# Kernel tuning notes

Measured on AMD Instinct MI355X. Metric: run time of the kernel, lower is better.

The kernel has to match this reference:

```python
import jax, jax.numpy as jnp
import numpy as np

B = 16
H = 56
W = 56
C = 384
NH = 12
HD = C // NH
WS = 7
SHIFT = 3
N = WS * WS
SCALE = HD ** -0.5
EPS = 1e-3  # keras LayerNormalization default epsilon


def _rel_pos_index():
    coords = np.stack(np.meshgrid(np.arange(WS), np.arange(WS), indexing='ij')).reshape(2, -1)
    rel = (coords[:, :, None] - coords[:, None, :]).transpose(1, 2, 0)
    rel[:, :, 0] += WS - 1
    rel[:, :, 1] += WS - 1
    rel[:, :, 0] *= 2 * WS - 1
    return rel.sum(-1)  # [N, N]

REL_IDX = jnp.asarray(_rel_pos_index())


def _shift_mask():
    # faithful reproduction of the TransformerBlock.__init__ mask construction
    mask = np.zeros((1, H, W, 1), np.float32)
    slices = (slice(0, -WS), slice(-WS, -SHIFT), slice(-SHIFT, None))
    cnt = 0
    for hs in slices:
        for ws in slices:
            mask[:, hs, ws, :] = cnt
            cnt += 1
    mw = mask.reshape(1, H // WS, WS, W // WS, WS, 1).transpose(0, 1, 3, 2, 4, 5).reshape(-1, N)
    m = mw[:, None, :] - mw[:, :, None]  # expand_dims(mw,1) - expand_dims(mw,2)
    return np.where(m != 0, np.float32(-100.0), np.float32(0.0))  # [nw, N, N]

MASK = jnp.asarray(_shift_mask())


def _ln(x, g, b):
    mu = x.mean(-1, keepdims=True)
    var = ((x - mu) ** 2).mean(-1, keepdims=True)
    return (x - mu) / jnp.sqrt(var + EPS) * g + b


def _window_partition(x):  # [B,H,W,C] -> [B*nw, N, C]
    b = x.shape[0]
    x = x.reshape(b, H // WS, WS, W // WS, WS, C).transpose(0, 1, 3, 2, 4, 5)
    return x.reshape(-1, N, C)


def _window_reverse(wins, b):  # [B*nw, WS, WS, C] -> [B,H,W,C]
    x = wins.reshape(b, H // WS, W // WS, WS, WS, C).transpose(0, 1, 3, 2, 4, 5)
    return x.reshape(b, H, W, C)


def setup_inputs() -> dict:
    key = jax.random.key(0)
    ks = jax.random.split(key, 8)
    s = 0.02
    return {
        'x': jax.random.normal(ks[0], (B, H * W, C), jnp.float32),
        'ln1_g': jnp.ones((C,), jnp.float32),
        'ln1_b': jnp.zeros((C,), jnp.float32),
        'ln2_g': jnp.ones((C,), jnp.float32),
        'ln2_b': jnp.zeros((C,), jnp.float32),
        'qkv_w': s * jax.random.normal(ks[1], (C, 3 * C), jnp.float32),
        'qkv_b': jnp.zeros((3 * C,), jnp.float32),
        'proj_w': s * jax.random.normal(ks[2], (C, C), jnp.float32),
        'proj_b': jnp.zeros((C,), jnp.float32),
        'mlp_w1': s * jax.random.normal(ks[3], (C, 4 * C), jnp.float32),
        'mlp_b1': jnp.zeros((4 * C,), jnp.float32),
        'mlp_w2': s * jax.random.normal(ks[4], (4 * C, C), jnp.float32),
        'mlp_b2': jnp.zeros((C,), jnp.float32),
        'rel_pos_table': s * jax.random.normal(ks[5], ((2 * WS - 1) * (2 * WS - 1), NH), jnp.float32),
    }


def reference(x, ln1_g, ln1_b, ln2_g, ln2_b, qkv_w, qkv_b, proj_w, proj_b,
              mlp_w1, mlp_b1, mlp_w2, mlp_b2, rel_pos_table):
    skip = x
    y = _ln(x, ln1_g, ln1_b).reshape(B, H, W, C)
    # cyclic shift (faithful to source: shift=(-s, +s))
    y = jnp.roll(y, shift=(-SHIFT, SHIFT), axis=(1, 2))
    wins = _window_partition(y)                      # [nW, N, C]
    nW = wins.shape[0]

    qkv = wins @ qkv_w + qkv_b                       # [nW, N, 3C]
    qkv = qkv.reshape(nW, N, 3, NH, HD).transpose(2, 0, 3, 1, 4)
    q, k, v = qkv[0] * SCALE, qkv[1], qkv[2]         # [nW, NH, N, HD]

    attn = jnp.einsum('whnd,whmd->whnm', q, k)       # [nW, NH, N, N]
    bias = rel_pos_table[REL_IDX.reshape(-1)].reshape(N, N, NH).transpose(2, 0, 1)
    attn = attn + bias[None]

    nw = MASK.shape[0]
    attn = attn.reshape(nW // nw, nw, NH, N, N) + MASK[None, :, None]
    attn = jax.nn.softmax(attn.reshape(nW, NH, N, N), axis=-1)

    out = jnp.einsum('whnm,whmd->wnhd', attn, v).reshape(nW, N, C)
    out = out @ proj_w + proj_b

    y = _window_reverse(out.reshape(-1, WS, WS, C), B)
    # reverse shift (faithful to source: shift=(+s, +s))
    y = jnp.roll(y, shift=(SHIFT, SHIFT), axis=(1, 2))
    x = y.reshape(B, H * W, C) + skip

    skip = x
    y = _ln(x, ln2_g, ln2_b)
    y = jax.nn.gelu(y @ mlp_w1 + mlp_b1, approximate=False)
    y = y @ mlp_w2 + mlp_b2
    return y + skip
```

## Files before the change

### kernel.cpp

```cpp
#include <hip/hip_runtime.h>
#include <hip/hip_bf16.h>
#include <math.h>

typedef __hip_bfloat16 bf16;
typedef unsigned short ushort_t;
typedef __bf16 bf16x8 __attribute__((ext_vector_type(8)));
typedef float f32x4 __attribute__((ext_vector_type(4)));

#define TOKENS 50176
#define CW2 512
#define CROWS2 (CW2 * 49)
#define SCALE_ 0.17677669529663687f

__device__ __forceinline__ float b2f(bf16 v) { return __bfloat162float(v); }
__device__ __forceinline__ bf16  f2b(float v) { return __float2bfloat16(v); }

__device__ __forceinline__ float gelu_f(float v) {
  float x = v * 0.7071067811865475f;
  float ax = fabsf(x);
  float t = 1.f / (1.f + 0.3275911f * ax);
  float poly = ((((1.061405429f * t - 1.453152027f) * t + 1.421413741f) * t
                 - 0.284496736f) * t + 0.254829592f) * t;
  float erfv = 1.f - poly * __expf(-ax * ax);
  erfv = copysignf(erfv, x);
  return 0.5f * v * (1.f + erfv);
}

__global__ __launch_bounds__(256) void wt_bf16(const float* __restrict__ W,
                                               ushort_t* __restrict__ Wt,
                                               int K, int N) {
  int idx = blockIdx.x * 256 + threadIdx.x;
  if (idx >= K * N) return;
  int n = idx / K, k = idx - n * K;
  bf16 h = f2b(W[(size_t)k * N + n]);
  Wt[idx] = *(ushort_t*)&h;
}

__global__ __launch_bounds__(64) void ln1_kernel(const float* __restrict__ x,
                                                 const float* __restrict__ g,
                                                 const float* __restrict__ bta,
                                                 bf16* __restrict__ wins) {
  int t = blockIdx.x;
  int lane = threadIdx.x;
  int w = t / 49, n = t - w * 49;
  int bi = w >> 6, wi = w & 63;
  int hw = wi >> 3, ww = wi & 7;
  int ti = n / 7, tj = n - ti * 7;
  int hr = hw * 7 + ti, wr = ww * 7 + tj;
  int hs = (hr + 3) % 56;
  int wsc = (wr + 53) % 56;
  const float* row = x + ((size_t)bi * 3136 + hs * 56 + wsc) * 384;
  float v[6];
  float s = 0.f, s2 = 0.f;
#pragma unroll
  for (int j = 0; j < 6; ++j) {
    v[j] = row[lane + 64 * j];
    s += v[j]; s2 += v[j] * v[j];
  }
#pragma unroll
  for (int m = 32; m >= 1; m >>= 1) {
    s  += __shfl_xor(s, m, 64);
    s2 += __shfl_xor(s2, m, 64);
  }
  float mu = s * (1.f / 384.f);
  float var = s2 * (1.f / 384.f) - mu * mu;
  float rstd = rsqrtf(var + 1e-3f);
  bf16* orow = wins + (size_t)t * 384;
#pragma unroll
  for (int j = 0; j < 6; ++j) {
    int c = lane + 64 * j;
    orow[c] = f2b((v[j] - mu) * rstd * g[c] + bta[c]);
  }
}

__global__ __launch_bounds__(64) void ln2_kernel(const float* __restrict__ x1,
                                                 const float* __restrict__ g,
                                                 const float* __restrict__ bta,
                                                 bf16* __restrict__ out) {
  int t = blockIdx.x;
  int lane = threadIdx.x;
  const float* row = x1 + (size_t)t * 384;
  float v[6];
  float s = 0.f, s2 = 0.f;
#pragma unroll
  for (int j = 0; j < 6; ++j) {
    v[j] = row[lane + 64 * j];
    s += v[j]; s2 += v[j] * v[j];
  }
#pragma unroll
  for (int m = 32; m >= 1; m >>= 1) {
    s  += __shfl_xor(s, m, 64);
    s2 += __shfl_xor(s2, m, 64);
  }
  float mu = s * (1.f / 384.f);
  float var = s2 * (1.f / 384.f) - mu * mu;
  float rstd = rsqrtf(var + 1e-3f);
  bf16* orow = out + (size_t)t * 384;
#pragma unroll
  for (int j = 0; j < 6; ++j) {
    int c = lane + 64 * j;
    orow[c] = f2b((v[j] - mu) * rstd * g[c] + bta[c]);
  }
}

template<int MODE>
__global__ __launch_bounds__(256) void mfma_gemm(
    const ushort_t* __restrict__ A, const ushort_t* __restrict__ Bt,
    const float* __restrict__ bias, int N, int K,
    const float* __restrict__ resid, void* __restrict__ out_) {
  __shared__ ushort_t As[2][128 * 32];
  __shared__ ushort_t Bs[2][128 * 32];
  int tid = threadIdx.x;
  int lane = tid & 63, wv = tid >> 6;
  int wm = wv >> 1, wn = wv & 1;
  int lm = lane & 15, kg = lane >> 4;
  int col0 = blockIdx.x * 128, row0 = blockIdx.y * 128;
  f32x4 acc[4][4];
#pragma unroll
  for (int i = 0; i < 4; ++i)
#pragma unroll
    for (int j = 0; j < 4; ++j) acc[i][j] = (f32x4){0.f, 0.f, 0.f, 0.f};

  int rsub = lane >> 2;
  int bs = (lane & 3) ^ ((rsub >> 1) & 3);
  int pbr = kg ^ ((lm >> 1) & 3);

  auto stage = [&](int t, int buf) {
    int kk0 = t << 5;
#pragma unroll
    for (int ch = 0; ch < 2; ++ch) {
      int c = wv * 2 + ch;
      int r = c * 16 + rsub;
      const ushort_t* ga = &A[(size_t)(row0 + r) * K + kk0 + bs * 8];
      const ushort_t* gb = &Bt[(size_t)(col0 + r) * K + kk0 + bs * 8];
      __builtin_amdgcn_global_load_lds(
          (const __attribute__((address_space(1))) void*)ga,
          (__attribute__((address_space(3))) void*)&As[buf][c * 512], 16, 0, 0);
      __builtin_amdgcn_global_load_lds(
          (const __attribute__((address_space(1))) void*)gb,
          (__attribute__((address_space(3))) void*)&Bs[buf][c * 512], 16, 0, 0);
    }
  };

  int NT = K >> 5;
  int cur = 0;
  stage(0, 0);
  __syncthreads();

  for (int t = 0; t < NT; ++t) {
    if (t + 1 < NT) stage(t + 1, cur ^ 1);
    bf16x8 a[4], b[4];
#pragma unroll
    for (int i = 0; i < 4; ++i) {
      int ra = wm * 64 + i * 16 + lm;
      int rb = wn * 64 + i * 16 + lm;
      a[i] = *(const bf16x8*)&As[cur][ra * 32 + pbr * 8];
      b[i] = *(const bf16x8*)&Bs[cur][rb * 32 + pbr * 8];
    }
#pragma unroll
    for (int i = 0; i < 4; ++i)
#pragma unroll
      for (int j = 0; j < 4; ++j)
        acc[i][j] = __builtin_amdgcn_mfma_f32_16x16x32_bf16(a[i], b[j], acc[i][j], 0, 0, 0);
    __syncthreads();
    cur ^= 1;
  }

  int m0 = row0 + wm * 64, n0 = col0 + wn * 64;
#pragma unroll
  for (int i = 0; i < 4; ++i) {
#pragma unroll
    for (int reg = 0; reg < 4; ++reg) {
      int m = m0 + i * 16 + kg * 4 + reg;
      size_t obase = 0;
      if (MODE == 1) {
        int w = m / 49, nn = m - w * 49;
        int bi = w >> 6, wi = w & 63;
        int hw = wi >> 3, ww = wi & 7;
        int ti = nn / 7, tj = nn - ti * 7;
        int hf = (hw * 7 + ti + 3) % 56, wf = (ww * 7 + tj + 3) % 56;
        obase = ((size_t)bi * 3136 + hf * 56 + wf) * 384;
      }
#pragma unroll
      for (int j = 0; j < 4; ++j) {
        int cN = n0 + j * 16 + lm;
        float v = acc[i][j][reg] + bias[cN];
        if (MODE == 0) {
          ((bf16*)out_)[(size_t)m * N + cN] = f2b(v);
        } else if (MODE == 1) {
          float* O = (float*)out_;
          O[obase + cN] = v + resid[obase + cN];
        } else if (MODE == 2) {
          ((bf16*)out_)[(size_t)m * N + cN] = f2b(gelu_f(v));
        } else {
          float* O = (float*)out_;
          O[(size_t)m * N + cN] = v + resid[(size_t)m * N + cN];
        }
      }
    }
  }
}

__global__ __launch_bounds__(256) void attn_mfma(const ushort_t* __restrict__ qkv_c,
                                                 const float* __restrict__ table,
                                                 ushort_t* __restrict__ attn_c,
                                                 int w_base) {
  int wl = blockIdx.x >> 2, hg = blockIdx.x & 3;
  int w = w_base + wl;
  int wi = w & 63;
  int hw = wi >> 3, ww = wi & 7;
  __shared__ ushort_t Qs[64 * 40];
  __shared__ ushort_t Ks[64 * 40];
  __shared__ ushort_t Vt[32 * 72];
  __shared__ ushort_t Ps[64 * 72];
  __shared__ float bias_s[169 * 12];
  int tid = threadIdx.x;
  int lane = tid & 63, wv = tid >> 6;
  int lm = lane & 15, kg = lane >> 4;

  for (int i = tid; i < 64 * 40; i += 256) { Qs[i] = 0; Ks[i] = 0; }
  for (int i = tid; i < 32 * 72; i += 256) Vt[i] = 0;
  for (int i = tid; i < 169 * 12; i += 256) bias_s[i] = table[i];
  __syncthreads();

  for (int hh = 0; hh < 3; ++hh) {
    int h = hg * 3 + hh;
    const ushort_t* base = qkv_c + (size_t)wl * 49 * 1152 + h * 32;
    for (int idx = tid; idx < 392; idx += 256) {
      int n = idx >> 3, d0 = (idx & 7) * 4;
      const ushort_t* p = base + (size_t)n * 1152 + d0;
      ushort4 q = *(const ushort4*)(p);
      ushort4 k = *(const ushort4*)(p + 384);
      ushort4 v = *(const ushort4*)(p + 768);
      *(ushort4*)&Qs[n * 40 + d0] = q;
      *(ushort4*)&Ks[n * 40 + d0] = k;
      Vt[(d0 + 0) * 72 + n] = v.x;
      Vt[(d0 + 1) * 72 + n] = v.y;
      Vt[(d0 + 2) * 72 + n] = v.z;
      Vt[(d0 + 3) * 72 + n] = v.w;
    }
    __syncthreads();

    bf16x8 qa = *(const bf16x8*)&Qs[(wv * 16 + lm) * 40 + kg * 8];
    f32x4 sacc[4];
#pragma unroll
    for (int jt = 0; jt < 4; ++jt) {
      bf16x8 kb = *(const bf16x8*)&Ks[(jt * 16 + lm) * 40 + kg * 8];
      sacc[jt] = __builtin_amdgcn_mfma_f32_16x16x32_bf16(
          qa, kb, (f32x4){0.f, 0.f, 0.f, 0.f}, 0, 0, 0);
    }

    int i_base = wv * 16 + kg * 4;
#pragma unroll
    for (int reg = 0; reg < 4; ++reg) {
      int i = i_base + reg;
      int ii = (i < 49) ? i : 0;
      int yi = ii / 7, xi = ii - yi * 7;
      int hri = hw * 7 + yi, wri = ww * 7 + xi;
      int ri = (hri < 49 ? 0 : (hri < 53 ? 1 : 2)) * 3 + (wri < 49 ? 0 : (wri < 53 ? 1 : 2));
      float sv[4];
      float mx = -1e30f;
#pragma unroll
      for (int jt = 0; jt < 4; ++jt) {
        int j = jt * 16 + lm;
        int jj = (j < 49) ? j : 0;
        int yj = jj / 7, xj = jj - yj * 7;
        int hrj = hw * 7 + yj, wrj = ww * 7 + xj;
        int rj = (hrj < 49 ? 0 : (hrj < 53 ? 1 : 2)) * 3 + (wrj < 49 ? 0 : (wrj < 53 ? 1 : 2));
        int ridx = (yi - yj + 6) * 13 + (xi - xj + 6);
        float s = sacc[jt][reg] * SCALE_ + bias_s[ridx * 12 + h] + ((ri == rj) ? 0.f : -100.f);
        sv[jt] = (j < 49) ? s : -1e30f;
        mx = fmaxf(mx, sv[jt]);
      }
#pragma unroll
      for (int msk = 1; msk < 16; msk <<= 1) mx = fmaxf(mx, __shfl_xor(mx, msk, 64));
      float sm = 0.f;
#pragma unroll
      for (int jt = 0; jt < 4; ++jt) {
        float e = ((jt * 16 + lm) < 49) ? __expf(sv[jt] - mx) : 0.f;
        sv[jt] = e; sm += e;
      }
#pragma unroll
      for (int msk = 1; msk < 16; msk <<= 1) sm += __shfl_xor(sm, msk, 64);
      float inv = 1.f / sm;
#pragma unroll
      for (int jt = 0; jt < 4; ++jt) {
        bf16 pb = f2b(sv[jt] * inv);
        Ps[(size_t)i * 72 + jt * 16 + lm] = *(ushort_t*)&pb;
      }
    }
    f32x4 oacc[2] = {(f32x4){0.f, 0.f, 0.f, 0.f}, (f32x4){0.f, 0.f, 0.f, 0.f}};
#pragma unroll
    for (int ks = 0; ks < 2; ++ks) {
      bf16x8 pa = *(const bf16x8*)&Ps[(wv * 16 + lm) * 72 + ks * 32 + kg * 8];
#pragma unroll
      for (int dt = 0; dt < 2; ++dt) {
        bf16x8 vb = *(const bf16x8*)&Vt[(dt * 16 + lm) * 72 + ks * 32 + kg * 8];
        oacc[dt] = __builtin_amdgcn_mfma_f32_16x16x32_bf16(pa, vb, oacc[dt], 0, 0, 0);
      }
    }
#pragma unroll
    for (int reg = 0; reg < 4; ++reg) {
      int r = i_base + reg;
      if (r < 49) {
#pragma unroll
        for (int dt = 0; dt < 2; ++dt) {
          bf16 ob = f2b(oacc[dt][reg]);
          attn_c[((size_t)wl * 49 + r) * 384 + h * 32 + dt * 16 + lm] = *(ushort_t*)&ob;
        }
      }
    }
    __syncthreads();
  }
}

extern "C" void kernel_launch(void* const* d_in, const int* in_sizes, int n_in,
                              void* d_out, int out_size, void* d_ws, size_t ws_size,
                              hipStream_t stream) {
  const float* x      = (const float*)d_in[0];
  const float* ln1_g  = (const float*)d_in[1];
  const float* ln1_b  = (const float*)d_in[2];
  const float* ln2_g  = (const float*)d_in[3];
  const float* ln2_b  = (const float*)d_in[4];
  const float* qkv_w  = (const float*)d_in[5];
  const float* qkv_b  = (const float*)d_in[6];
  const float* proj_w = (const float*)d_in[7];
  const float* proj_b = (const float*)d_in[8];
  const float* mlp_w1 = (const float*)d_in[9];
  const float* mlp_b1 = (const float*)d_in[10];
  const float* mlp_w2 = (const float*)d_in[11];
  const float* mlp_b2 = (const float*)d_in[12];
  const float* rel_tb = (const float*)d_in[13];

  char* ws = (char*)d_ws;
  ushort_t* r0 = (ushort_t*)(ws + 0);
  ushort_t* r1 = (ushort_t*)(ws + 38535168ull);
  ushort_t* wq = (ushort_t*)(ws + 115605504ull);
  ushort_t* wp = wq + 442368;
  ushort_t* w1 = wp + 147456;
  ushort_t* w2 = w1 + 589824;
  float* out = (float*)d_out;

  wt_bf16<<<1728, 256, 0, stream>>>(qkv_w, wq, 384, 1152);
  wt_bf16<<<576, 256, 0, stream>>>(proj_w, wp, 384, 384);
  wt_bf16<<<2304, 256, 0, stream>>>(mlp_w1, w1, 384, 1536);
  wt_bf16<<<2304, 256, 0, stream>>>(mlp_w2, w2, 1536, 384);

  ln1_kernel<<<TOKENS, 64, 0, stream>>>(x, ln1_g, ln1_b, (bf16*)r0);

  for (int c = 0; c < 2; ++c) {
    ushort_t* winc = r0 + (size_t)c * CROWS2 * 384;
    mfma_gemm<0><<<dim3(9, CROWS2 / 128), 256, 0, stream>>>(
        winc, wq, qkv_b, 1152, 384, nullptr, (void*)r1);
    attn_mfma<<<CW2 * 4, 256, 0, stream>>>(r1, rel_tb, winc, c * CW2);
  }

  mfma_gemm<1><<<dim3(3, TOKENS / 128), 256, 0, stream>>>(
      r0, wp, proj_b, 384, 384, x, (void*)out);

  ln2_kernel<<<TOKENS, 64, 0, stream>>>(out, ln2_g, ln2_b, (bf16*)r0);

  for (int c = 0; c < 2; ++c) {
    ushort_t* lc = r0 + (size_t)c * CROWS2 * 384;
    float* oc = out + (size_t)c * CROWS2 * 384;
    mfma_gemm<2><<<dim3(12, CROWS2 / 128), 256, 0, stream>>>(
        lc, w1, mlp_b1, 1536, 384, nullptr, (void*)r1);
    mfma_gemm<3><<<dim3(3, CROWS2 / 128), 256, 0, stream>>>(
        r1, w2, mlp_b2, 384, 1536, oc, (void*)oc);
  }
}
```

Measured before the change: 668.5 us.

## Triple-buffer GEMM LDS pipeline and remap blocks for XCD-aware locality

The MFMA GEMM moves from a double-buffered to a triple-buffered LDS pipeline. Loads are issued two K-tiles ahead, and it waits with a partial vmcnt instead of draining, so there is one barrier per iteration. Launch now uses a 1D grid, and block IDs are remapped so consecutive tiles land on the same XCD, which is meant to improve L2 reuse of the shared A rows. The costs are 50% more LDS per block, which may lower occupancy, and reliance on hand-tuned waitcnt counts.

```diff
diff --git a/kernel.cpp b/kernel.cpp
--- a/kernel.cpp
+++ b/kernel.cpp
@@ -108,13 +108,20 @@
     const ushort_t* __restrict__ A, const ushort_t* __restrict__ Bt,
     const float* __restrict__ bias, int N, int K,
     const float* __restrict__ resid, void* __restrict__ out_) {
-  __shared__ ushort_t As[2][128 * 32];
-  __shared__ ushort_t Bs[2][128 * 32];
+  __shared__ ushort_t As[3][128 * 32];
+  __shared__ ushort_t Bs[3][128 * 32];
   int tid = threadIdx.x;
   int lane = tid & 63, wv = tid >> 6;
   int wm = wv >> 1, wn = wv & 1;
   int lm = lane & 15, kg = lane >> 4;
-  int col0 = blockIdx.x * 128, row0 = blockIdx.y * 128;
+
+  int nwg = gridDim.x;
+  int q = nwg >> 3, r = nwg & 7;
+  int xcd = blockIdx.x & 7, ii = blockIdx.x >> 3;
+  int l = ((xcd < r) ? xcd * (q + 1) : r * (q + 1) + (xcd - r) * q) + ii;
+  int nxt = N >> 7;
+  int col0 = (l % nxt) * 128, row0 = (l / nxt) * 128;
+
   f32x4 acc[4][4];
 #pragma unroll
   for (int i = 0; i < 4; ++i)
@@ -122,7 +129,7 @@
     for (int j = 0; j < 4; ++j) acc[i][j] = (f32x4){0.f, 0.f, 0.f, 0.f};
 
   int rsub = lane >> 2;
-  int bs = (lane & 3) ^ ((rsub >> 1) & 3);
+  int bsrc = (lane & 3) ^ ((rsub >> 1) & 3);
   int pbr = kg ^ ((lm >> 1) & 3);
 
   auto stage = [&](int t, int buf) {
@@ -130,9 +137,9 @@
 #pragma unroll
     for (int ch = 0; ch < 2; ++ch) {
       int c = wv * 2 + ch;
-      int r = c * 16 + rsub;
-      const ushort_t* ga = &A[(size_t)(row0 + r) * K + kk0 + bs * 8];
-      const ushort_t* gb = &Bt[(size_t)(col0 + r) * K + kk0 + bs * 8];
+      int rr = c * 16 + rsub;
+      const ushort_t* ga = &A[(size_t)(row0 + rr) * K + kk0 + bsrc * 8];
+      const ushort_t* gb = &Bt[(size_t)(col0 + rr) * K + kk0 + bsrc * 8];
       __builtin_amdgcn_global_load_lds(
           (const __attribute__((address_space(1))) void*)ga,
           (__attribute__((address_space(3))) void*)&As[buf][c * 512], 16, 0, 0);
@@ -142,29 +149,37 @@
     }
   };
 
-  int NT = K >> 5;
-  int cur = 0;
-  stage(0, 0);
-  __syncthreads();
-
-  for (int t = 0; t < NT; ++t) {
-    if (t + 1 < NT) stage(t + 1, cur ^ 1);
+  auto compute = [&](int buf) {
     bf16x8 a[4], b[4];
 #pragma unroll
     for (int i = 0; i < 4; ++i) {
       int ra = wm * 64 + i * 16 + lm;
       int rb = wn * 64 + i * 16 + lm;
-      a[i] = *(const bf16x8*)&As[cur][ra * 32 + pbr * 8];
-      b[i] = *(const bf16x8*)&Bs[cur][rb * 32 + pbr * 8];
+      a[i] = *(const bf16x8*)&As[buf][ra * 32 + pbr * 8];
+      b[i] = *(const bf16x8*)&Bs[buf][rb * 32 + pbr * 8];
     }
 #pragma unroll
     for (int i = 0; i < 4; ++i)
 #pragma unroll
       for (int j = 0; j < 4; ++j)
         acc[i][j] = __builtin_amdgcn_mfma_f32_16x16x32_bf16(a[i], b[j], acc[i][j], 0, 0, 0);
-    __syncthreads();
-    cur ^= 1;
-  }
+  };
+
+  int NT = K >> 5;
+  stage(0, 0);
+  stage(1, 1);
+
+  for (int t = 0; t < NT - 1; ++t) {
+    asm volatile("s_waitcnt vmcnt(4)" ::: "memory");
+    __builtin_amdgcn_sched_barrier(0);
+    __builtin_amdgcn_s_barrier();
+    if (t + 2 < NT) stage(t + 2, (t + 2) % 3);
+    compute(t % 3);
+  }
+  asm volatile("s_waitcnt vmcnt(0)" ::: "memory");
+  __builtin_amdgcn_sched_barrier(0);
+  __builtin_amdgcn_s_barrier();
+  compute((NT - 1) % 3);
 
   int m0 = row0 + wm * 64, n0 = col0 + wn * 64;
 #pragma unroll
@@ -350,12 +365,12 @@
 
   for (int c = 0; c < 2; ++c) {
     ushort_t* winc = r0 + (size_t)c * CROWS2 * 384;
-    mfma_gemm<0><<<dim3(9, CROWS2 / 128), 256, 0, stream>>>(
+    mfma_gemm<0><<<9 * (CROWS2 / 128), 256, 0, stream>>>(
         winc, wq, qkv_b, 1152, 384, nullptr, (void*)r1);
     attn_mfma<<<CW2 * 4, 256, 0, stream>>>(r1, rel_tb, winc, c * CW2);
   }
 
-  mfma_gemm<1><<<dim3(3, TOKENS / 128), 256, 0, stream>>>(
+  mfma_gemm<1><<<3 * (TOKENS / 128), 256, 0, stream>>>(
       r0, wp, proj_b, 384, 384, x, (void*)out);
 
   ln2_kernel<<<TOKENS, 64, 0, stream>>>(out, ln2_g, ln2_b, (bf16*)r0);
@@ -363,9 +378,9 @@
   for (int c = 0; c < 2; ++c) {
     ushort_t* lc = r0 + (size_t)c * CROWS2 * 384;
     float* oc = out + (size_t)c * CROWS2 * 384;
-    mfma_gemm<2><<<dim3(12, CROWS2 / 128), 256, 0, stream>>>(
+    mfma_gemm<2><<<12 * (CROWS2 / 128), 256, 0, stream>>>(
         lc, w1, mlp_b1, 1536, 384, nullptr, (void*)r1);
-    mfma_gemm<3><<<dim3(3, CROWS2 / 128), 256, 0, stream>>>(
+    mfma_gemm<3><<<3 * (CROWS2 / 128), 256, 0, stream>>>(
         r1, w2, mlp_b2, 384, 1536, oc, (void*)oc);
   }
 }
```

After: 686.0 us. 1.03x slower.

## Use 512-thread single-buffered GEMM blocks with XCD-aware tile remapping

Applied to the files above, without the earlier changes.

The MFMA GEMM now runs 8 waves per 128x128 tile, each computing 32x64 instead of 64x64, so per-thread accumulators halve and more waves fit per CU. LDS double buffering is dropped in favour of a single buffer with a sync after each load, relying on the higher occupancy to hide latency. Tiles are launched on a 1D grid and remapped so consecutive tiles land on the same XCD, to improve L2 reuse. The load-then-sync pattern loses any overlap inside a block, which can hurt if occupancy does not actually rise.

```diff
diff --git a/kernel.cpp b/kernel.cpp
--- a/kernel.cpp
+++ b/kernel.cpp
@@ -104,71 +104,68 @@
 }
 
 template<int MODE>
-__global__ __launch_bounds__(256) void mfma_gemm(
+__global__ __launch_bounds__(512, 6) void mfma_gemm(
     const ushort_t* __restrict__ A, const ushort_t* __restrict__ Bt,
     const float* __restrict__ bias, int N, int K,
     const float* __restrict__ resid, void* __restrict__ out_) {
-  __shared__ ushort_t As[2][128 * 32];
-  __shared__ ushort_t Bs[2][128 * 32];
+  __shared__ ushort_t As[128 * 32];
+  __shared__ ushort_t Bs[128 * 32];
   int tid = threadIdx.x;
   int lane = tid & 63, wv = tid >> 6;
   int wm = wv >> 1, wn = wv & 1;
   int lm = lane & 15, kg = lane >> 4;
-  int col0 = blockIdx.x * 128, row0 = blockIdx.y * 128;
-  f32x4 acc[4][4];
-#pragma unroll
-  for (int i = 0; i < 4; ++i)
+
+  int nwg = gridDim.x;
+  int q = nwg >> 3, r = nwg & 7;
+  int xcd = blockIdx.x & 7, ii = blockIdx.x >> 3;
+  int l = ((xcd < r) ? xcd * (q + 1) : r * (q + 1) + (xcd - r) * q) + ii;
+  int nxt = N >> 7;
+  int col0 = (l % nxt) * 128, row0 = (l / nxt) * 128;
+
+  f32x4 acc[2][4];
+#pragma unroll
+  for (int i = 0; i < 2; ++i)
 #pragma unroll
     for (int j = 0; j < 4; ++j) acc[i][j] = (f32x4){0.f, 0.f, 0.f, 0.f};
 
   int rsub = lane >> 2;
-  int bs = (lane & 3) ^ ((rsub >> 1) & 3);
+  int bsrc = (lane & 3) ^ ((rsub >> 1) & 3);
   int pbr = kg ^ ((lm >> 1) & 3);
 
-  auto stage = [&](int t, int buf) {
-    int kk0 = t << 5;
-#pragma unroll
-    for (int ch = 0; ch < 2; ++ch) {
-      int c = wv * 2 + ch;
-      int r = c * 16 + rsub;
-      const ushort_t* ga = &A[(size_t)(row0 + r) * K + kk0 + bs * 8];
-      const ushort_t* gb = &Bt[(size_t)(col0 + r) * K + kk0 + bs * 8];
-      __builtin_amdgcn_global_load_lds(
-          (const __attribute__((address_space(1))) void*)ga,
-          (__attribute__((address_space(3))) void*)&As[buf][c * 512], 16, 0, 0);
-      __builtin_amdgcn_global_load_lds(
-          (const __attribute__((address_space(1))) void*)gb,
-          (__attribute__((address_space(3))) void*)&Bs[buf][c * 512], 16, 0, 0);
-    }
-  };
+  const ushort_t* gA = &A[(size_t)(row0 + wv * 16 + rsub) * K + bsrc * 8];
+  const ushort_t* gB = &Bt[(size_t)(col0 + wv * 16 + rsub) * K + bsrc * 8];
 
   int NT = K >> 5;
-  int cur = 0;
-  stage(0, 0);
-  __syncthreads();
-
   for (int t = 0; t < NT; ++t) {
-    if (t + 1 < NT) stage(t + 1, cur ^ 1);
-    bf16x8 a[4], b[4];
-#pragma unroll
-    for (int i = 0; i < 4; ++i) {
-      int ra = wm * 64 + i * 16 + lm;
-      int rb = wn * 64 + i * 16 + lm;
-      a[i] = *(const bf16x8*)&As[cur][ra * 32 + pbr * 8];
-      b[i] = *(const bf16x8*)&Bs[cur][rb * 32 + pbr * 8];
-    }
-#pragma unroll
-    for (int i = 0; i < 4; ++i)
+    __builtin_amdgcn_global_load_lds(
+        (const __attribute__((address_space(1))) void*)(gA + (t << 5)),
+        (__attribute__((address_space(3))) void*)&As[wv * 512], 16, 0, 0);
+    __builtin_amdgcn_global_load_lds(
+        (const __attribute__((address_space(1))) void*)(gB + (t << 5)),
+        (__attribute__((address_space(3))) void*)&Bs[wv * 512], 16, 0, 0);
+    __syncthreads();
+    bf16x8 a[2], b[4];
+#pragma unroll
+    for (int i = 0; i < 2; ++i) {
+      int ra = wm * 32 + i * 16 + lm;
+      a[i] = *(const bf16x8*)&As[ra * 32 + pbr * 8];
+    }
+#pragma unroll
+    for (int j = 0; j < 4; ++j) {
+      int rb = wn * 64 + j * 16 + lm;
+      b[j] = *(const bf16x8*)&Bs[rb * 32 + pbr * 8];
+    }
+#pragma unroll
+    for (int i = 0; i < 2; ++i)
 #pragma unroll
       for (int j = 0; j < 4; ++j)
         acc[i][j] = __builtin_amdgcn_mfma_f32_16x16x32_bf16(a[i], b[j], acc[i][j], 0, 0, 0);
     __syncthreads();
-    cur ^= 1;
-  }
-
-  int m0 = row0 + wm * 64, n0 = col0 + wn * 64;
-#pragma unroll
-  for (int i = 0; i < 4; ++i) {
+  }
+
+  int m0 = row0 + wm * 32, n0 = col0 + wn * 64;
+#pragma unroll
+  for (int i = 0; i < 2; ++i) {
 #pragma unroll
     for (int reg = 0; reg < 4; ++reg) {
       int m = m0 + i * 16 + kg * 4 + reg;
@@ -350,12 +347,12 @@
 
   for (int c = 0; c < 2; ++c) {
     ushort_t* winc = r0 + (size_t)c * CROWS2 * 384;
-    mfma_gemm<0><<<dim3(9, CROWS2 / 128), 256, 0, stream>>>(
+    mfma_gemm<0><<<(CROWS2 / 128) * 9, 512, 0, stream>>>(
         winc, wq, qkv_b, 1152, 384, nullptr, (void*)r1);
     attn_mfma<<<CW2 * 4, 256, 0, stream>>>(r1, rel_tb, winc, c * CW2);
   }
 
-  mfma_gemm<1><<<dim3(3, TOKENS / 128), 256, 0, stream>>>(
+  mfma_gemm<1><<<(TOKENS / 128) * 3, 512, 0, stream>>>(
       r0, wp, proj_b, 384, 384, x, (void*)out);
 
   ln2_kernel<<<TOKENS, 64, 0, stream>>>(out, ln2_g, ln2_b, (bf16*)r0);
@@ -363,9 +360,9 @@
   for (int c = 0; c < 2; ++c) {
     ushort_t* lc = r0 + (size_t)c * CROWS2 * 384;
     float* oc = out + (size_t)c * CROWS2 * 384;
-    mfma_gemm<2><<<dim3(12, CROWS2 / 128), 256, 0, stream>>>(
+    mfma_gemm<2><<<(CROWS2 / 128) * 12, 512, 0, stream>>>(
         lc, w1, mlp_b1, 1536, 384, nullptr, (void*)r1);
-    mfma_gemm<3><<<dim3(3, CROWS2 / 128), 256, 0, stream>>>(
+    mfma_gemm<3><<<(CROWS2 / 128) * 3, 512, 0, stream>>>(
         r1, w2, mlp_b2, 384, 1536, oc, (void*)oc);
   }
 }
```

Measured after the change: 600.2 us. -10.2%, faster.
